# Kernel optimization log

Hardware: AMD Instinct MI355X
Metric: run time of the kernel (lower is better)

The kernel has to match this reference:

```python
import jax, jax.numpy as jnp
import numpy as np

N = 100000
E = 1600000
IN_DIM = 128
H = 64
OUT_DIM = 64
EPS = 1e-5


def batch_norm(x, gamma, beta):
    # BatchNorm1d with batch statistics (training-mode normalization, biased var)
    mu = jnp.mean(x, axis=0)
    var = jnp.var(x, axis=0)
    return (x - mu) * jax.lax.rsqrt(var + EPS) * gamma + beta


def gcn_conv(x, src, dst, W, b, n_nodes):
    # PyG GCNConv: add self-loops, symmetric deg^-1/2 normalization, X W, scatter-add, bias
    loop = jnp.arange(n_nodes, dtype=src.dtype)
    s = jnp.concatenate([src, loop])
    d = jnp.concatenate([dst, loop])
    w = jnp.ones(s.shape[0], dtype=x.dtype)
    deg = jax.ops.segment_sum(w, d, num_segments=n_nodes)
    dinv = jnp.where(deg > 0, jax.lax.rsqrt(deg), 0.0)
    norm = dinv[s] * w * dinv[d]                      # [E+N]
    h = x @ W                                         # [N, out]
    msg = h[s] * norm[:, None]                        # [E+N, out]
    out = jax.ops.segment_sum(msg, d, num_segments=n_nodes)
    return out + b


def setup_inputs() -> dict:
    key = jax.random.key(0)
    ks = jax.random.split(key, 12)
    x = jax.random.normal(ks[0], (N, IN_DIM), dtype=jnp.float32)
    edge_index = jax.random.randint(ks[1], (2, E), 0, N, dtype=jnp.int64)
    s = 0.05
    return {
        "x": x,
        "edge_index": edge_index,
        "bn_in_g": jnp.ones((IN_DIM,), jnp.float32),
        "bn_in_b": jnp.zeros((IN_DIM,), jnp.float32),
        "Wp": jax.random.normal(ks[2], (IN_DIM, H), jnp.float32) * s,
        "bp": jnp.zeros((H,), jnp.float32),
        "W1": jax.random.normal(ks[3], (H, H), jnp.float32) * s,
        "b1": jnp.zeros((H,), jnp.float32),
        "bn1_g": jnp.ones((H,), jnp.float32),
        "bn1_b": jnp.zeros((H,), jnp.float32),
        "W2": jax.random.normal(ks[4], (H, OUT_DIM), jnp.float32) * s,
        "b2": jnp.zeros((OUT_DIM,), jnp.float32),
        "bn2_g": jnp.ones((OUT_DIM,), jnp.float32),
        "bn2_b": jnp.zeros((OUT_DIM,), jnp.float32),
    }


def reference(x, edge_index, bn_in_g, bn_in_b, Wp, bp, W1, b1, bn1_g, bn1_b, W2, b2, bn2_g, bn2_b):
    src, dst = edge_index[0], edge_index[1]
    n = x.shape[0]
    h0 = batch_norm(x, bn_in_g, bn_in_b)
    h0 = jax.nn.relu(h0 @ Wp + bp)
    h1 = gcn_conv(h0, src, dst, W1, b1, n)
    h1 = jax.nn.relu(batch_norm(h1, bn1_g, bn1_b))
    # dropout in eval mode: identity
    h2 = gcn_conv(h1, src, dst, W2, b2, n)
    return batch_norm(h2, bn2_g, bn2_b)
```

## Files before the change

### kernel.cpp

```cpp
#include <hip/hip_runtime.h>
#include <hip/hip_bf16.h>

#define EPS 1e-5f
#define CAP 6144
#define PCHUNK 4096

__device__ __forceinline__ void acc_q(float* acc, uint2 v, float s) {
    acc[0] += s * (float)((int)(v.x << 24) >> 24);
    acc[1] += s * (float)((int)(v.x << 16) >> 24);
    acc[2] += s * (float)((int)(v.x << 8) >> 24);
    acc[3] += s * (float)((int)v.x >> 24);
    acc[4] += s * (float)((int)(v.y << 24) >> 24);
    acc[5] += s * (float)((int)(v.y << 16) >> 24);
    acc[6] += s * (float)((int)(v.y << 8) >> 24);
    acc[7] += s * (float)((int)v.y >> 24);
}

__global__ void k_init(int* __restrict__ cur, float* __restrict__ stats) {
    int t = threadIdx.x;
    stats[t] = 0.0f;
    cur[t] = t * CAP;
}

__global__ __launch_bounds__(256) void k_A(
    const int* __restrict__ src, const int* __restrict__ dst,
    int* __restrict__ cur, unsigned* __restrict__ packbuf, int E, int NBP,
    const float* __restrict__ x, float* __restrict__ xsum, float* __restrict__ xsq, int N) {
    __shared__ int h[512], delta[512], wsc[4];
    __shared__ unsigned buf[PCHUNK];
    __shared__ int addr[PCHUNK];
    int tx = threadIdx.x;
    if ((int)blockIdx.x < NBP) {
        int e0 = blockIdx.x * PCHUNK;
        int e1 = min(e0 + PCHUNK, E);
        int csize = e1 - e0;
        h[tx] = 0; h[tx + 256] = 0;
        __syncthreads();
        for (int e = e0 + tx; e < e1; e += 256)
            atomicAdd(&h[dst[e] >> 8], 1);
        __syncthreads();
        int b0 = tx * 2;
        int c0 = h[b0], c1 = h[b0 + 1];
        int tsum = c0 + c1;
        int lane = tx & 63, wid = tx >> 6;
        int v = tsum;
#pragma unroll
        for (int off = 1; off < 64; off <<= 1) {
            int u = __shfl_up(v, off);
            if (lane >= off) v += u;
        }
        if (lane == 63) wsc[wid] = v;
        __syncthreads();
        int wbase = 0;
        for (int w = 0; w < wid; w++) wbase += wsc[w];
        int excl0 = wbase + v - tsum;
        int excl1 = excl0 + c0;
        if (c0 > 0) delta[b0] = atomicAdd(&cur[b0], c0) - excl0;
        if (c1 > 0) delta[b0 + 1] = atomicAdd(&cur[b0 + 1], c1) - excl1;
        __syncthreads();
        h[b0] = excl0; h[b0 + 1] = excl1;
        __syncthreads();
        for (int e = e0 + tx; e < e1; e += 256) {
            int d = dst[e];
            int b = d >> 8;
            int rank = atomicAdd(&h[b], 1);
            buf[rank] = ((unsigned)src[e] << 8) | (unsigned)(d & 255);
            addr[rank] = delta[b];
        }
        __syncthreads();
        for (int i = tx; i < csize; i += 256)
            packbuf[addr[i] + i] = buf[i];
    } else {
        float* ls = (float*)buf;
        float* lq = ls + 256;
        int b2 = blockIdx.x - NBP;
        int col = tx & 127, half = tx >> 7;
        float s = 0.f, q = 0.f;
        for (int r = b2 * 2 + half; r < N; r += 1024) {
            float v = x[(long long)r * 128 + col];
            s += v; q += v * v;
        }
        ls[tx] = s; lq[tx] = q;
        __syncthreads();
        if (half == 0) {
            s = ls[tx] + ls[tx + 128];
            q = lq[tx] + lq[tx + 128];
            atomicAdd(&xsum[col], s);
            atomicAdd(&xsq[col], q);
        }
    }
}

__global__ __launch_bounds__(512) void k_B(
    const unsigned* __restrict__ packbuf, const int* __restrict__ cur,
    int2* __restrict__ rowbe, int* __restrict__ rowmid, float* __restrict__ dinv,
    int* __restrict__ eidx, int NB, int N, int Nh,
    const float* __restrict__ x, const float* __restrict__ stats,
    const float* __restrict__ g, const float* __restrict__ bbn,
    const float* __restrict__ Wp, const float* __restrict__ bp,
    float* __restrict__ H, float invN) {
    __shared__ int cnt[512], loff[512], wsum[8];
    int tx = threadIdx.x;
    if ((int)blockIdx.x < NB) {
        int b = blockIdx.x;
        int base = b * CAP;
        int end = cur[b];
        cnt[tx] = 0;
        __syncthreads();
        for (int e = base + tx; e < end; e += 512) {
            unsigned pk = packbuf[e];
            int key = (((int)pk & 255) << 1) | (int)((pk >> 8) >= (unsigned)Nh);
            atomicAdd(&cnt[key], 1);
        }
        __syncthreads();
        int c = cnt[tx];
        int lane = tx & 63, wid = tx >> 6;
        int v = c;
#pragma unroll
        for (int off = 1; off < 64; off <<= 1) {
            int u = __shfl_up(v, off);
            if (lane >= off) v += u;
        }
        if (lane == 63) wsum[wid] = v;
        __syncthreads();
        int wbase = 0;
        for (int w = 0; w < wid; w++) wbase += wsum[w];
        int excl = wbase + v - c;
        loff[tx] = excl;
        __syncthreads();
        if (tx < 256) {
            int node = b * 256 + tx;
            if (node < N) {
                int beg = base + loff[2 * tx];
                int mid = base + loff[2 * tx + 1];
                int e2 = mid + cnt[2 * tx + 1];
                rowbe[node] = make_int2(beg, e2);
                rowmid[node] = mid;
                int deg = cnt[2 * tx] + cnt[2 * tx + 1];
                dinv[node] = rsqrtf(1.0f + (float)deg);
            }
        }
        __syncthreads();
        for (int e = base + tx; e < end; e += 512) {
            unsigned pk = packbuf[e];
            int key = (((int)pk & 255) << 1) | (int)((pk >> 8) >= (unsigned)Nh);
            int pos = atomicAdd(&loff[key], 1);
            eidx[base + pos] = (int)(pk >> 8);
        }
    } else {
        float* sc = (float*)cnt;
        float* sh = (float*)loff;
        if (tx < 128) {
            float mu = stats[tx] * invN;
            float var = stats[128 + tx] * invN - mu * mu;
            float s = g[tx] * rsqrtf(var + EPS);
            sc[tx] = s;
            sh[tx] = bbn[tx] - mu * s;
        }
        __syncthreads();
        int r = ((int)blockIdx.x - NB) * 512 + tx;
        if (r >= N) return;
        float acc[64];
#pragma unroll
        for (int j = 0; j < 64; j++) acc[j] = 0.f;
        const float4* x4 = (const float4*)(x + (long long)r * 128);
        for (int c4 = 0; c4 < 32; c4++) {
            float4 xv = x4[c4];
            int cb = c4 * 4;
            xv.x = xv.x * sc[cb + 0] + sh[cb + 0];
            xv.y = xv.y * sc[cb + 1] + sh[cb + 1];
            xv.z = xv.z * sc[cb + 2] + sh[cb + 2];
            xv.w = xv.w * sc[cb + 3] + sh[cb + 3];
#pragma unroll
            for (int q = 0; q < 4; q++) {
                float xs = (q == 0) ? xv.x : (q == 1) ? xv.y : (q == 2) ? xv.z : xv.w;
                const float* wrow = Wp + (c4 * 4 + q) * 64;
#pragma unroll
                for (int j = 0; j < 64; j++) acc[j] += xs * wrow[j];
            }
        }
        float4* out4 = (float4*)(H + (long long)r * 64);
#pragma unroll
        for (int i = 0; i < 16; i++) {
            float4 vv;
            vv.x = fmaxf(acc[4 * i + 0] + bp[4 * i + 0], 0.f);
            vv.y = fmaxf(acc[4 * i + 1] + bp[4 * i + 1], 0.f);
            vv.z = fmaxf(acc[4 * i + 2] + bp[4 * i + 2], 0.f);
            vv.w = fmaxf(acc[4 * i + 3] + bp[4 * i + 3], 0.f);
            out4[i] = vv;
        }
    }
}

template <bool BNRELU>
__global__ __launch_bounds__(256) void k_gemm_scale(
    const float* __restrict__ In, const float* __restrict__ W,
    const float* __restrict__ dinv, const float* __restrict__ ssum,
    const float* __restrict__ ssq, const float* __restrict__ g,
    const float* __restrict__ bb, float invN, unsigned* __restrict__ Bq,
    float* __restrict__ S, int N) {
    __shared__ float scs[64], shs[64];
    int tx = threadIdx.x;
    if (BNRELU) {
        if (tx < 64) {
            float mu = ssum[tx] * invN;
            float var = ssq[tx] * invN - mu * mu;
            float s = g[tx] * rsqrtf(var + EPS);
            scs[tx] = s;
            shs[tx] = bb[tx] - mu * s;
        }
        __syncthreads();
    }
    int r = blockIdx.x * blockDim.x + tx;
    if (r >= N) return;
    float acc[64];
#pragma unroll
    for (int j = 0; j < 64; j++) acc[j] = 0.f;
    const float4* in4 = (const float4*)(In + (long long)r * 64);
    for (int c4 = 0; c4 < 16; c4++) {
        float4 xv = in4[c4];
        if (BNRELU) {
            int cb = c4 * 4;
            xv.x = fmaxf(xv.x * scs[cb + 0] + shs[cb + 0], 0.f);
            xv.y = fmaxf(xv.y * scs[cb + 1] + shs[cb + 1], 0.f);
            xv.z = fmaxf(xv.z * scs[cb + 2] + shs[cb + 2], 0.f);
            xv.w = fmaxf(xv.w * scs[cb + 3] + shs[cb + 3], 0.f);
        }
#pragma unroll
        for (int q = 0; q < 4; q++) {
            float xs = (q == 0) ? xv.x : (q == 1) ? xv.y : (q == 2) ? xv.z : xv.w;
            const float* wrow = W + (c4 * 4 + q) * 64;
#pragma unroll
            for (int j = 0; j < 64; j++) acc[j] += xs * wrow[j];
        }
    }
    float dv = dinv[r];
    float vmax = 0.f;
#pragma unroll
    for (int j = 0; j < 64; j++) {
        acc[j] *= dv;
        vmax = fmaxf(vmax, fabsf(acc[j]));
    }
    S[r] = vmax * (1.0f / 127.0f);
    float inv = (vmax > 0.f) ? (127.0f / vmax) : 0.f;
    uint4* b4 = (uint4*)(Bq + (long long)r * 16);
#pragma unroll
    for (int i = 0; i < 4; i++) {
        unsigned w[4];
#pragma unroll
        for (int k2 = 0; k2 < 4; k2++) {
            int bsx = i * 16 + k2 * 4;
            unsigned q0 = (unsigned)((int)rintf(acc[bsx + 0] * inv)) & 255u;
            unsigned q1 = (unsigned)((int)rintf(acc[bsx + 1] * inv)) & 255u;
            unsigned q2 = (unsigned)((int)rintf(acc[bsx + 2] * inv)) & 255u;
            unsigned q3 = (unsigned)((int)rintf(acc[bsx + 3] * inv)) & 255u;
            w[k2] = q0 | (q1 << 8) | (q2 << 16) | (q3 << 24);
        }
        b4[i] = make_uint4(w[0], w[1], w[2], w[3]);
    }
}

__global__ __launch_bounds__(256) void k_gather_finish(
    const uint2* __restrict__ B, const float* __restrict__ S,
    const int2* __restrict__ rowbe, const int* __restrict__ rowmid,
    const int* __restrict__ eidx,
    const float* __restrict__ dinv, const float* __restrict__ bias,
    float* __restrict__ Out, float* __restrict__ ssum, float* __restrict__ ssq,
    int N, int Nh) {
    int tx = threadIdx.x;
    int g = tx >> 3;
    int l = tx & 7;
    int d = blockIdx.x * 32 + g;

    float s[8], q[8];
#pragma unroll
    for (int j = 0; j < 8; j++) { s[j] = 0.f; q[j] = 0.f; }

    if (d < N) {
        int2 be = rowbe[d];
        int mid = rowmid[d];
        uint2 v0 = B[(long long)d * 8 + l];
        float sd = S[d];
        float dv = dinv[d];

        float acc[8];
#pragma unroll
        for (int j = 0; j < 8; j++) acc[j] = 0.f;

        for (int seg = 0; seg < 2; seg++) {
            int k  = seg ? mid : be.x;
            int ke = seg ? be.y : mid;
            if (k >= ke) continue;
            int dmy = seg ? Nh : 0;
            int idx_cur[8];
#pragma unroll
            for (int j = 0; j < 8; j++)
                idx_cur[j] = (k + j < ke) ? eidx[k + j] : dmy;

            while (k < ke) {
                uint2 bb[8];
                float sv[8];
#pragma unroll
                for (int j = 0; j < 8; j++)
                    bb[j] = B[(long long)idx_cur[j] * 8 + l];
#pragma unroll
                for (int j = 0; j < 8; j++)
                    sv[j] = (k + j < ke) ? S[idx_cur[j]] : 0.f;
                int kn = k + 8;
                int idx_nxt[8];
#pragma unroll
                for (int j = 0; j < 8; j++)
                    idx_nxt[j] = (kn + j < ke) ? eidx[kn + j] : dmy;
#pragma unroll
                for (int j = 0; j < 8; j++)
                    acc_q(acc, bb[j], sv[j]);
#pragma unroll
                for (int j = 0; j < 8; j++) idx_cur[j] = idx_nxt[j];
                k = kn;
            }
        }
        acc_q(acc, v0, sd);

        float4 o0, o1;
#pragma unroll
        for (int j = 0; j < 8; j++) {
            float v = acc[j] * dv + bias[8 * l + j];
            ((j < 4) ? (&o0.x)[j] : (&o1.x)[j - 4]) = v;
            s[j] += v; q[j] += v * v;
        }
        float4* outp = (float4*)(Out + (long long)d * 64 + 8 * l);
        outp[0] = o0;
        outp[1] = o1;
    }

#pragma unroll
    for (int m = 8; m <= 32; m <<= 1) {
#pragma unroll
        for (int j = 0; j < 8; j++) {
            s[j] += __shfl_xor(s[j], m, 64);
            q[j] += __shfl_xor(q[j], m, 64);
        }
    }
    __shared__ float ws_s[4][64], ws_q[4][64];
    int wv = tx >> 6, ln = tx & 63;
    if (ln < 8) {
#pragma unroll
        for (int j = 0; j < 8; j++) {
            ws_s[wv][ln * 8 + j] = s[j];
            ws_q[wv][ln * 8 + j] = q[j];
        }
    }
    __syncthreads();
    if (tx < 64) {
        float S2 = ws_s[0][tx] + ws_s[1][tx] + ws_s[2][tx] + ws_s[3][tx];
        float Q2 = ws_q[0][tx] + ws_q[1][tx] + ws_q[2][tx] + ws_q[3][tx];
        atomicAdd(&ssum[tx], S2);
        atomicAdd(&ssq[tx], Q2);
    }
}

__global__ __launch_bounds__(256) void k_final(const float* __restrict__ In,
                                               const float* __restrict__ ssum,
                                               const float* __restrict__ ssq,
                                               const float* __restrict__ g,
                                               const float* __restrict__ bb, float invN,
                                               float* __restrict__ out, int total4) {
    __shared__ float scs[64], shs[64];
    int tx = threadIdx.x;
    if (tx < 64) {
        float mu = ssum[tx] * invN;
        float var = ssq[tx] * invN - mu * mu;
        float s = g[tx] * rsqrtf(var + EPS);
        scs[tx] = s;
        shs[tx] = bb[tx] - mu * s;
    }
    __syncthreads();
    int t = blockIdx.x * blockDim.x + tx;
    if (t < total4) {
        float4 v = ((const float4*)In)[t];
        int j = (t * 4) & 63;
        v.x = v.x * scs[j + 0] + shs[j + 0];
        v.y = v.y * scs[j + 1] + shs[j + 1];
        v.z = v.z * scs[j + 2] + shs[j + 2];
        v.w = v.w * scs[j + 3] + shs[j + 3];
        ((float4*)out)[t] = v;
    }
}

extern "C" void kernel_launch(void* const* d_in, const int* in_sizes, int n_in,
                              void* d_out, int out_size, void* d_ws, size_t ws_size,
                              hipStream_t stream) {
    const float* x       = (const float*)d_in[0];
    const int*   ei      = (const int*)d_in[1];
    const float* bn_in_g = (const float*)d_in[2];
    const float* bn_in_b = (const float*)d_in[3];
    const float* Wp      = (const float*)d_in[4];
    const float* bp      = (const float*)d_in[5];
    const float* W1      = (const float*)d_in[6];
    const float* b1      = (const float*)d_in[7];
    const float* bn1_g   = (const float*)d_in[8];
    const float* bn1_b   = (const float*)d_in[9];
    const float* W2      = (const float*)d_in[10];
    const float* b2      = (const float*)d_in[11];
    const float* bn2_g   = (const float*)d_in[12];
    const float* bn2_b   = (const float*)d_in[13];

    int N = in_sizes[0] / 128;
    int E = in_sizes[1] / 2;
    const int* src = ei;
    const int* dst = ei + E;
    int Nh  = N >> 1;
    int NB  = (N + 255) >> 8;
    int NBP = (E + PCHUNK - 1) / PCHUNK;
    int nbg = (N + 511) / 512;

    long long Npad = ((long long)N + 128) & ~127LL;
    int*   cur    = (int*)d_ws;
    float* stats  = (float*)(cur + 512);
    int2*  rowbe  = (int2*)(stats + 512);
    float* dinv   = (float*)(rowbe + Npad);
    int*   rowmid = (int*)(dinv + Npad);
    float* S      = (float*)(rowmid + Npad);
    unsigned* packbuf = (unsigned*)(S + Npad);
    int*   eidx   = (int*)(packbuf + (long long)NB * CAP);
    unsigned* Bq  = (unsigned*)(eidx + (long long)NB * CAP);
    float* H      = (float*)d_out;

    int nb = (N + 255) / 256;
    int gb = (N + 31) / 32;
    float invN = 1.0f / (float)N;

    k_init<<<1, 512, 0, stream>>>(cur, stats);
    k_A<<<NBP + 512, 256, 0, stream>>>(src, dst, cur, packbuf, E, NBP,
                                       x, stats, stats + 128, N);
    k_B<<<NB + nbg, 512, 0, stream>>>(packbuf, cur, rowbe, rowmid, dinv, eidx, NB, N, Nh,
                                      x, stats, bn_in_g, bn_in_b, Wp, bp, H, invN);

    k_gemm_scale<false><<<nb, 256, 0, stream>>>(H, W1, dinv, nullptr, nullptr, nullptr,
                                                nullptr, invN, Bq, S, N);
    k_gather_finish<<<gb, 256, 0, stream>>>((const uint2*)Bq, S, rowbe, rowmid, eidx, dinv,
                                            b1, H, stats + 256, stats + 320, N, Nh);

    k_gemm_scale<true><<<nb, 256, 0, stream>>>(H, W2, dinv, stats + 256, stats + 320,
                                               bn1_g, bn1_b, invN, Bq, S, N);
    k_gather_finish<<<gb, 256, 0, stream>>>((const uint2*)Bq, S, rowbe, rowmid, eidx, dinv,
                                            b2, H, stats + 384, stats + 448, N, Nh);

    k_final<<<(N * 16 + 255) / 256, 256, 0, stream>>>(H, stats + 384, stats + 448,
                                                      bn2_g, bn2_b, invN, H, N * 16);
}
```

Baseline: 476.7 us.

## Replace per-thread row GEMMs with shared-memory tiled 4x4 register-blocked GEMMs

```diff
diff --git a/kernel.cpp b/kernel.cpp
--- a/kernel.cpp
+++ b/kernel.cpp
@@ -4,6 +4,7 @@
 #define EPS 1e-5f
 #define CAP 6144
 #define PCHUNK 4096
+#define XP 68
 
 __device__ __forceinline__ void acc_q(float* acc, uint2 v, float s) {
     acc[0] += s * (float)((int)(v.x << 24) >> 24);
@@ -99,9 +100,12 @@
     const float* __restrict__ g, const float* __restrict__ bbn,
     const float* __restrict__ Wp, const float* __restrict__ bp,
     float* __restrict__ H, float invN) {
-    __shared__ int cnt[512], loff[512], wsum[8];
+    __shared__ __align__(16) char smem[52224];
     int tx = threadIdx.x;
     if ((int)blockIdx.x < NB) {
+        int* cnt  = (int*)smem;
+        int* loff = cnt + 512;
+        int* wsum = loff + 512;
         int b = blockIdx.x;
         int base = b * CAP;
         int end = cur[b];
@@ -148,120 +152,192 @@
             eidx[base + pos] = (int)(pk >> 8);
         }
     } else {
-        float* sc = (float*)cnt;
-        float* sh = (float*)loff;
+        float* xs  = (float*)smem;
+        float* ws  = xs + 128 * XP;
+        float* scb = ws + 4096;
+        float* shb = scb + 128;
         if (tx < 128) {
             float mu = stats[tx] * invN;
             float var = stats[128 + tx] * invN - mu * mu;
             float s = g[tx] * rsqrtf(var + EPS);
-            sc[tx] = s;
-            sh[tx] = bbn[tx] - mu * s;
-        }
-        __syncthreads();
-        int r = ((int)blockIdx.x - NB) * 512 + tx;
-        if (r >= N) return;
-        float acc[64];
-#pragma unroll
-        for (int j = 0; j < 64; j++) acc[j] = 0.f;
-        const float4* x4 = (const float4*)(x + (long long)r * 128);
-        for (int c4 = 0; c4 < 32; c4++) {
-            float4 xv = x4[c4];
-            int cb = c4 * 4;
-            xv.x = xv.x * sc[cb + 0] + sh[cb + 0];
-            xv.y = xv.y * sc[cb + 1] + sh[cb + 1];
-            xv.z = xv.z * sc[cb + 2] + sh[cb + 2];
-            xv.w = xv.w * sc[cb + 3] + sh[cb + 3];
-#pragma unroll
-            for (int q = 0; q < 4; q++) {
-                float xs = (q == 0) ? xv.x : (q == 1) ? xv.y : (q == 2) ? xv.z : xv.w;
-                const float* wrow = Wp + (c4 * 4 + q) * 64;
-#pragma unroll
-                for (int j = 0; j < 64; j++) acc[j] += xs * wrow[j];
+            scb[tx] = s;
+            shb[tx] = bbn[tx] - mu * s;
+        }
+        __syncthreads();
+        int r0 = ((int)blockIdx.x - NB) * 128;
+        int cw = tx & 15, rw = tx >> 4;
+        float acc[4][4];
+#pragma unroll
+        for (int j = 0; j < 4; j++)
+#pragma unroll
+            for (int i = 0; i < 4; i++) acc[j][i] = 0.f;
+
+        for (int kc = 0; kc < 128; kc += 64) {
+#pragma unroll
+            for (int i = 0; i < 4; i++) {
+                int f = tx + 512 * i;
+                int row = f >> 4, kq = f & 15;
+                int rr = r0 + row;
+                float4 v = make_float4(0.f, 0.f, 0.f, 0.f);
+                if (rr < N) v = ((const float4*)(x + (long long)rr * 128 + kc))[kq];
+                int cb = kc + kq * 4;
+                v.x = v.x * scb[cb + 0] + shb[cb + 0];
+                v.y = v.y * scb[cb + 1] + shb[cb + 1];
+                v.z = v.z * scb[cb + 2] + shb[cb + 2];
+                v.w = v.w * scb[cb + 3] + shb[cb + 3];
+                *(float4*)&xs[row * XP + kq * 4] = v;
             }
-        }
-        float4* out4 = (float4*)(H + (long long)r * 64);
-#pragma unroll
-        for (int i = 0; i < 16; i++) {
-            float4 vv;
-            vv.x = fmaxf(acc[4 * i + 0] + bp[4 * i + 0], 0.f);
-            vv.y = fmaxf(acc[4 * i + 1] + bp[4 * i + 1], 0.f);
-            vv.z = fmaxf(acc[4 * i + 2] + bp[4 * i + 2], 0.f);
-            vv.w = fmaxf(acc[4 * i + 3] + bp[4 * i + 3], 0.f);
-            out4[i] = vv;
+#pragma unroll
+            for (int i = 0; i < 2; i++) {
+                int f = tx + 512 * i;
+                int k = f >> 4, cq = f & 15;
+                float4 w = ((const float4*)(Wp + (long long)(kc + k) * 64))[cq];
+                *(float4*)&ws[k * 64 + cq * 4] = w;
+            }
+            __syncthreads();
+#pragma unroll
+            for (int k4 = 0; k4 < 16; k4++) {
+                float xv[4][4], wv[4][4];
+#pragma unroll
+                for (int j = 0; j < 4; j++) {
+                    float4 v = *(const float4*)&xs[(rw * 4 + j) * XP + k4 * 4];
+                    xv[j][0] = v.x; xv[j][1] = v.y; xv[j][2] = v.z; xv[j][3] = v.w;
+                }
+#pragma unroll
+                for (int kk = 0; kk < 4; kk++) {
+                    float4 w = *(const float4*)&ws[(k4 * 4 + kk) * 64 + cw * 4];
+                    wv[kk][0] = w.x; wv[kk][1] = w.y; wv[kk][2] = w.z; wv[kk][3] = w.w;
+                }
+#pragma unroll
+                for (int kk = 0; kk < 4; kk++)
+#pragma unroll
+                    for (int j = 0; j < 4; j++)
+#pragma unroll
+                        for (int i = 0; i < 4; i++)
+                            acc[j][i] += xv[j][kk] * wv[kk][i];
+            }
+            __syncthreads();
+        }
+        float4 bpv = ((const float4*)bp)[cw];
+#pragma unroll
+        for (int j = 0; j < 4; j++) {
+            int rr = r0 + rw * 4 + j;
+            if (rr < N) {
+                float4 o;
+                o.x = fmaxf(acc[j][0] + bpv.x, 0.f);
+                o.y = fmaxf(acc[j][1] + bpv.y, 0.f);
+                o.z = fmaxf(acc[j][2] + bpv.z, 0.f);
+                o.w = fmaxf(acc[j][3] + bpv.w, 0.f);
+                ((float4*)(H + (long long)rr * 64))[cw] = o;
+            }
         }
     }
 }
 
 template <bool BNRELU>
-__global__ __launch_bounds__(256) void k_gemm_scale(
+__global__ __launch_bounds__(512) void k_gemm_scale(
     const float* __restrict__ In, const float* __restrict__ W,
     const float* __restrict__ dinv, const float* __restrict__ ssum,
     const float* __restrict__ ssq, const float* __restrict__ g,
     const float* __restrict__ bb, float invN, unsigned* __restrict__ Bq,
     float* __restrict__ S, int N) {
-    __shared__ float scs[64], shs[64];
+    __shared__ __align__(16) char smem[52224];
+    float* xs  = (float*)smem;
+    float* ws  = xs + 128 * XP;
+    float* scb = ws + 4096;
+    float* shb = scb + 128;
     int tx = threadIdx.x;
     if (BNRELU) {
         if (tx < 64) {
             float mu = ssum[tx] * invN;
             float var = ssq[tx] * invN - mu * mu;
             float s = g[tx] * rsqrtf(var + EPS);
-            scs[tx] = s;
-            shs[tx] = bb[tx] - mu * s;
-        }
-        __syncthreads();
-    }
-    int r = blockIdx.x * blockDim.x + tx;
-    if (r >= N) return;
-    float acc[64];
-#pragma unroll
-    for (int j = 0; j < 64; j++) acc[j] = 0.f;
-    const float4* in4 = (const float4*)(In + (long long)r * 64);
-    for (int c4 = 0; c4 < 16; c4++) {
-        float4 xv = in4[c4];
+            scb[tx] = s;
+            shb[tx] = bb[tx] - mu * s;
+        }
+        __syncthreads();
+    }
+    int r0 = blockIdx.x * 128;
+    int cw = tx & 15, rw = tx >> 4;
+#pragma unroll
+    for (int i = 0; i < 4; i++) {
+        int f = tx + 512 * i;
+        int row = f >> 4, kq = f & 15;
+        int rr = r0 + row;
+        float4 v = make_float4(0.f, 0.f, 0.f, 0.f);
+        if (rr < N) v = ((const float4*)(In + (long long)rr * 64))[kq];
         if (BNRELU) {
-            int cb = c4 * 4;
-            xv.x = fmaxf(xv.x * scs[cb + 0] + shs[cb + 0], 0.f);
-            xv.y = fmaxf(xv.y * scs[cb + 1] + shs[cb + 1], 0.f);
-            xv.z = fmaxf(xv.z * scs[cb + 2] + shs[cb + 2], 0.f);
-            xv.w = fmaxf(xv.w * scs[cb + 3] + shs[cb + 3], 0.f);
-        }
-#pragma unroll
-        for (int q = 0; q < 4; q++) {
-            float xs = (q == 0) ? xv.x : (q == 1) ? xv.y : (q == 2) ? xv.z : xv.w;
-            const float* wrow = W + (c4 * 4 + q) * 64;
-#pragma unroll
-            for (int j = 0; j < 64; j++) acc[j] += xs * wrow[j];
-        }
-    }
-    float dv = dinv[r];
-    float vmax = 0.f;
-#pragma unroll
-    for (int j = 0; j < 64; j++) {
-        acc[j] *= dv;
-        vmax = fmaxf(vmax, fabsf(acc[j]));
-    }
-    S[r] = vmax * (1.0f / 127.0f);
-    float inv = (vmax > 0.f) ? (127.0f / vmax) : 0.f;
-    uint4* b4 = (uint4*)(Bq + (long long)r * 16);
-#pragma unroll
-    for (int i = 0; i < 4; i++) {
-        unsigned w[4];
-#pragma unroll
-        for (int k2 = 0; k2 < 4; k2++) {
-            int bsx = i * 16 + k2 * 4;
-            unsigned q0 = (unsigned)((int)rintf(acc[bsx + 0] * inv)) & 255u;
-            unsigned q1 = (unsigned)((int)rintf(acc[bsx + 1] * inv)) & 255u;
-            unsigned q2 = (unsigned)((int)rintf(acc[bsx + 2] * inv)) & 255u;
-            unsigned q3 = (unsigned)((int)rintf(acc[bsx + 3] * inv)) & 255u;
-            w[k2] = q0 | (q1 << 8) | (q2 << 16) | (q3 << 24);
-        }
-        b4[i] = make_uint4(w[0], w[1], w[2], w[3]);
+            int cb = kq * 4;
+            v.x = fmaxf(v.x * scb[cb + 0] + shb[cb + 0], 0.f);
+            v.y = fmaxf(v.y * scb[cb + 1] + shb[cb + 1], 0.f);
+            v.z = fmaxf(v.z * scb[cb + 2] + shb[cb + 2], 0.f);
+            v.w = fmaxf(v.w * scb[cb + 3] + shb[cb + 3], 0.f);
+        }
+        *(float4*)&xs[row * XP + kq * 4] = v;
+    }
+#pragma unroll
+    for (int i = 0; i < 2; i++) {
+        int f = tx + 512 * i;
+        int k = f >> 4, cq = f & 15;
+        float4 w = ((const float4*)(W + (long long)k * 64))[cq];
+        *(float4*)&ws[k * 64 + cq * 4] = w;
+    }
+    __syncthreads();
+    float acc[4][4];
+#pragma unroll
+    for (int j = 0; j < 4; j++)
+#pragma unroll
+        for (int i = 0; i < 4; i++) acc[j][i] = 0.f;
+#pragma unroll
+    for (int k4 = 0; k4 < 16; k4++) {
+        float xv[4][4], wv[4][4];
+#pragma unroll
+        for (int j = 0; j < 4; j++) {
+            float4 v = *(const float4*)&xs[(rw * 4 + j) * XP + k4 * 4];
+            xv[j][0] = v.x; xv[j][1] = v.y; xv[j][2] = v.z; xv[j][3] = v.w;
+        }
+#pragma unroll
+        for (int kk = 0; kk < 4; kk++) {
+            float4 w = *(const float4*)&ws[(k4 * 4 + kk) * 64 + cw * 4];
+            wv[kk][0] = w.x; wv[kk][1] = w.y; wv[kk][2] = w.z; wv[kk][3] = w.w;
+        }
+#pragma unroll
+        for (int kk = 0; kk < 4; kk++)
+#pragma unroll
+            for (int j = 0; j < 4; j++)
+#pragma unroll
+                for (int i = 0; i < 4; i++)
+                    acc[j][i] += xv[j][kk] * wv[kk][i];
+    }
+#pragma unroll
+    for (int j = 0; j < 4; j++) {
+        int rr = r0 + rw * 4 + j;
+        float dv = (rr < N) ? dinv[rr] : 0.f;
+        float m = 0.f;
+#pragma unroll
+        for (int i = 0; i < 4; i++) {
+            acc[j][i] *= dv;
+            m = fmaxf(m, fabsf(acc[j][i]));
+        }
+#pragma unroll
+        for (int mask = 1; mask < 16; mask <<= 1)
+            m = fmaxf(m, __shfl_xor(m, mask, 64));
+        float inv = (m > 0.f) ? (127.0f / m) : 0.f;
+        if (rr < N) {
+            if (cw == 0) S[rr] = m * (1.0f / 127.0f);
+            int q0 = (int)rintf(acc[j][0] * inv);
+            int q1 = (int)rintf(acc[j][1] * inv);
+            int q2 = (int)rintf(acc[j][2] * inv);
+            int q3 = (int)rintf(acc[j][3] * inv);
+            unsigned w = ((unsigned)q0 & 255u) | (((unsigned)q1 & 255u) << 8) |
+                         (((unsigned)q2 & 255u) << 16) | (((unsigned)q3 & 255u) << 24);
+            Bq[(long long)rr * 16 + cw] = w;
+        }
     }
 }
 
 __global__ __launch_bounds__(256) void k_gather_finish(
-    const uint2* __restrict__ B, const float* __restrict__ S,
+    const uint2* __restrict__ Q, const float* __restrict__ S,
     const int2* __restrict__ rowbe, const int* __restrict__ rowmid,
     const int* __restrict__ eidx,
     const float* __restrict__ dinv, const float* __restrict__ bias,
@@ -279,7 +355,7 @@
     if (d < N) {
         int2 be = rowbe[d];
         int mid = rowmid[d];
-        uint2 v0 = B[(long long)d * 8 + l];
+        uint2 v0 = Q[(long long)d * 8 + l];
         float sd = S[d];
         float dv = dinv[d];
 
@@ -302,7 +378,7 @@
                 float sv[8];
 #pragma unroll
                 for (int j = 0; j < 8; j++)
-                    bb[j] = B[(long long)idx_cur[j] * 8 + l];
+                    bb[j] = Q[(long long)idx_cur[j] * 8 + l];
 #pragma unroll
                 for (int j = 0; j < 8; j++)
                     sv[j] = (k + j < ke) ? S[idx_cur[j]] : 0.f;
@@ -412,7 +488,7 @@
     int Nh  = N >> 1;
     int NB  = (N + 255) >> 8;
     int NBP = (E + PCHUNK - 1) / PCHUNK;
-    int nbg = (N + 511) / 512;
+    int ntg = (N + 127) / 128;
 
     long long Npad = ((long long)N + 128) & ~127LL;
     int*   cur    = (int*)d_ws;
@@ -426,23 +502,22 @@
     unsigned* Bq  = (unsigned*)(eidx + (long long)NB * CAP);
     float* H      = (float*)d_out;
 
-    int nb = (N + 255) / 256;
     int gb = (N + 31) / 32;
     float invN = 1.0f / (float)N;
 
     k_init<<<1, 512, 0, stream>>>(cur, stats);
     k_A<<<NBP + 512, 256, 0, stream>>>(src, dst, cur, packbuf, E, NBP,
                                        x, stats, stats + 128, N);
-    k_B<<<NB + nbg, 512, 0, stream>>>(packbuf, cur, rowbe, rowmid, dinv, eidx, NB, N, Nh,
+    k_B<<<NB + ntg, 512, 0, stream>>>(packbuf, cur, rowbe, rowmid, dinv, eidx, NB, N, Nh,
                                       x, stats, bn_in_g, bn_in_b, Wp, bp, H, invN);
 
-    k_gemm_scale<false><<<nb, 256, 0, stream>>>(H, W1, dinv, nullptr, nullptr, nullptr,
-                                                nullptr, invN, Bq, S, N);
+    k_gemm_scale<false><<<ntg, 512, 0, stream>>>(H, W1, dinv, nullptr, nullptr, nullptr,
+                                                 nullptr, invN, Bq, S, N);
     k_gather_finish<<<gb, 256, 0, stream>>>((const uint2*)Bq, S, rowbe, rowmid, eidx, dinv,
                                             b1, H, stats + 256, stats + 320, N, Nh);
 
-    k_gemm_scale<true><<<nb, 256, 0, stream>>>(H, W2, dinv, stats + 256, stats + 320,
-                                               bn1_g, bn1_b, invN, Bq, S, N);
+    k_gemm_scale<true><<<ntg, 512, 0, stream>>>(H, W2, dinv, stats + 256, stats + 320,
+                                                bn1_g, bn1_b, invN, Bq, S, N);
     k_gather_finish<<<gb, 256, 0, stream>>>((const uint2*)Bq, S, rowbe, rowmid, eidx, dinv,
                                             b2, H, stats + 384, stats + 448, N, Nh);
 
```

After: 961.1 us. 2.02x slower.
